# Kernel optimization log

Hardware: AMD Instinct MI355X
Metric: run time of the kernel (lower is better)

The kernel has to match this reference:

```python
import jax, jax.numpy as jnp
import numpy as np

N_NODES = 100000
N_EDGES = 1600000
N_GRAPHS = 64
DIMS = [(128, 128), (128, 128), (128, 64)]  # (in, out) per SAGEConv layer


def setup_inputs() -> dict:
    key = jax.random.key(0)
    ks = jax.random.split(key, 16)
    inp = {
        "x": jax.random.normal(ks[0], (N_NODES, DIMS[0][0]), dtype=jnp.float32),
        "edge_index": jax.random.randint(ks[1], (2, N_EDGES), 0, N_NODES, dtype=jnp.int64),
        "batch": jnp.sort(jax.random.randint(ks[2], (N_NODES,), 0, N_GRAPHS, dtype=jnp.int64)),
        "edge_attr": jax.random.normal(ks[3], (N_EDGES, 4), dtype=jnp.float32),
    }
    # SAGEConv params: lin_l (applied to mean-aggregated neighbors, has bias),
    # lin_r (applied to root/self features, no bias) -- PyG defaults.
    for i, (din, dout) in enumerate(DIMS):
        s = 1.0 / np.sqrt(din)
        inp[f"Wl{i}"] = jax.random.normal(ks[4 + 3 * i], (din, dout), dtype=jnp.float32) * s
        inp[f"Wr{i}"] = jax.random.normal(ks[5 + 3 * i], (din, dout), dtype=jnp.float32) * s
        inp[f"b{i}"] = jnp.zeros((dout,), dtype=jnp.float32)
    return inp


def _sage_conv(x, edge_index, Wl, Wr, b):
    # messages flow src -> dst (PyG source_to_target), mean aggregation at dst
    src, dst = edge_index[0], edge_index[1]
    msg = x[src]  # [E, F] gather
    agg = jax.ops.segment_sum(msg, dst, num_segments=x.shape[0])  # [N, F]
    deg = jax.ops.segment_sum(jnp.ones((src.shape[0],), x.dtype), dst, num_segments=x.shape[0])
    agg = agg / jnp.maximum(deg, 1.0)[:, None]  # mean; isolated nodes -> 0
    return agg @ Wl + x @ Wr + b


def reference(x, edge_index, batch, edge_attr, Wl0, Wr0, b0, Wl1, Wr1, b1, Wl2, Wr2, b2):
    del edge_attr  # cast to float in original, never used by SAGEConv
    h = x.astype(jnp.float32)
    params = [(Wl0, Wr0, b0), (Wl1, Wr1, b1), (Wl2, Wr2, b2)]
    for i, (Wl, Wr, b) in enumerate(params):
        h = _sage_conv(h, edge_index, Wl, Wr, b)
        if i < len(params) - 1:
            h = jax.nn.relu(h)  # dropout is identity in eval mode
    # global_mean_pool over graphs
    pooled = jax.ops.segment_sum(h, batch, num_segments=N_GRAPHS)
    counts = jax.ops.segment_sum(jnp.ones((h.shape[0],), h.dtype), batch, num_segments=N_GRAPHS)
    return pooled / jnp.maximum(counts, 1.0)[:, None]
```

## Files before the change

### kernel.cpp

```cpp
#include <hip/hip_runtime.h>
#include <hip/hip_bf16.h>

#define NN 100000
#define NE 1600000
#define NG 64
#define NBUK 782
#define ABLK 512
#define ACH 3125
#define PSPLIT 8

typedef short short8 __attribute__((ext_vector_type(8)));
typedef float f32x4 __attribute__((ext_vector_type(4)));
typedef float f32x2 __attribute__((ext_vector_type(2)));
typedef unsigned short ushort8v __attribute__((ext_vector_type(8)));
typedef unsigned int uint4v __attribute__((ext_vector_type(4)));
typedef unsigned int uint2v __attribute__((ext_vector_type(2)));

static inline int cdiv(int a, int b) { return (a + b - 1) / b; }

__device__ __forceinline__ short f2bf(float f) {
    return __builtin_bit_cast(short, __float2bfloat16(f));
}
__device__ __forceinline__ float bf2f(unsigned short u) {
    unsigned int x = ((unsigned int)u) << 16;
    return __builtin_bit_cast(float, x);
}

__global__ __launch_bounds__(256) void histA_kernel(const int* __restrict__ dst,
                                                    int* __restrict__ blockHist, int E) {
    __shared__ int h[NBUK];
    for (int i = threadIdx.x; i < NBUK; i += 256) h[i] = 0;
    __syncthreads();
    int base = blockIdx.x * ACH;
    int end = min(base + ACH, E);
    for (int e = base + threadIdx.x; e < end; e += 256) atomicAdd(&h[dst[e] >> 7], 1);
    __syncthreads();
    for (int i = threadIdx.x; i < NBUK; i += 256) blockHist[(size_t)i * ABLK + blockIdx.x] = h[i];
}

__global__ __launch_bounds__(512) void scanBlk_kernel(int* __restrict__ blockHist,
                                                      int* __restrict__ bucketTot) {
    __shared__ int s[ABLK];
    int b = blockIdx.x, t = threadIdx.x;
    int v = blockHist[(size_t)b * ABLK + t];
    s[t] = v;
    __syncthreads();
    for (int o = 1; o < ABLK; o <<= 1) {
        int u = (t >= o) ? s[t - o] : 0;
        __syncthreads();
        s[t] += u;
        __syncthreads();
    }
    blockHist[(size_t)b * ABLK + t] = s[t] - v;
    if (t == ABLK - 1) bucketTot[b] = s[ABLK - 1];
}

__global__ __launch_bounds__(1024) void scanTot_kernel(const int* __restrict__ bucketTot,
                                                       int* __restrict__ bucketBase,
                                                       int* __restrict__ off, int E) {
    __shared__ int s[1024];
    int t = threadIdx.x;
    int v = (t < NBUK) ? bucketTot[t] : 0;
    s[t] = v;
    __syncthreads();
    for (int o = 1; o < 1024; o <<= 1) {
        int u = (t >= o) ? s[t - o] : 0;
        __syncthreads();
        s[t] += u;
        __syncthreads();
    }
    if (t < NBUK) bucketBase[t] = s[t] - v;
    if (t == 0) {
        bucketBase[NBUK] = E;
        off[NN] = E;
    }
}

__global__ __launch_bounds__(256) void binA_kernel(const int* __restrict__ src,
                                                   const int* __restrict__ dst,
                                                   const int* __restrict__ blockHist,
                                                   const int* __restrict__ bucketBase,
                                                   int* __restrict__ binned, int E) {
    __shared__ int cur[NBUK];
    __shared__ int lbase[NBUK];
    for (int i = threadIdx.x; i < NBUK; i += 256) {
        cur[i] = 0;
        lbase[i] = bucketBase[i] + blockHist[(size_t)i * ABLK + blockIdx.x];
    }
    __syncthreads();
    int base = blockIdx.x * ACH;
    int end = min(base + ACH, E);
    for (int e = base + threadIdx.x; e < end; e += 256) {
        int d = dst[e];
        int b = d >> 7;
        int r = atomicAdd(&cur[b], 1);
        binned[lbase[b] + r] = src[e] | ((d & 127) << 20);
    }
}

__global__ __launch_bounds__(256) void bucketB_kernel(const int* __restrict__ binned,
                                                      const int* __restrict__ bucketBase,
                                                      int* __restrict__ csr,
                                                      int* __restrict__ off,
                                                      float* __restrict__ ideg, int N) {
    __shared__ int pair[2048];
    __shared__ int stage[4096];
    __shared__ int deg[128], loff[128], cur[128];
    int b = blockIdx.x, t = threadIdx.x;
    int e0 = bucketBase[b], e1 = bucketBase[b + 1];
    int cnt = e1 - e0;
    if (t < 128) deg[t] = 0;
    __syncthreads();
    for (int c0 = 0; c0 < cnt; c0 += 2048) {
        int cc = min(2048, cnt - c0);
        for (int i = t; i < cc; i += 256) pair[i] = binned[e0 + c0 + i];
        __syncthreads();
        for (int i = t; i < cc; i += 256) atomicAdd(&deg[pair[i] >> 20], 1);
        __syncthreads();
    }
    if (t < 128) loff[t] = deg[t];
    __syncthreads();
    for (int o = 1; o < 128; o <<= 1) {
        int u = (t < 128 && t >= o) ? loff[t - o] : 0;
        __syncthreads();
        if (t < 128) loff[t] += u;
        __syncthreads();
    }
    int nodeBase = b * 128;
    if (t < 128) {
        int ex = loff[t] - deg[t];
        cur[t] = ex;
        int n = nodeBase + t;
        if (n < N) {
            off[n] = e0 + ex;
            ideg[n] = 1.0f / (float)max(deg[t], 1);
        }
    }
    __syncthreads();
    if (cnt <= 4096) {
        for (int c0 = 0; c0 < cnt; c0 += 2048) {
            int cc = min(2048, cnt - c0);
            for (int i = t; i < cc; i += 256) pair[i] = binned[e0 + c0 + i];
            __syncthreads();
            for (int i = t; i < cc; i += 256) {
                int p = pair[i];
                int r = atomicAdd(&cur[p >> 20], 1);
                stage[r] = p & 0xFFFFF;
            }
            __syncthreads();
        }
        for (int i = t; i < cnt; i += 256) csr[e0 + i] = stage[i];
    } else {
        for (int c0 = 0; c0 < cnt; c0 += 2048) {
            int cc = min(2048, cnt - c0);
            for (int i = t; i < cc; i += 256) pair[i] = binned[e0 + c0 + i];
            __syncthreads();
            for (int i = t; i < cc; i += 256) {
                int p = pair[i];
                int r = atomicAdd(&cur[p >> 20], 1);
                csr[e0 + r] = p & 0xFFFFF;
            }
            __syncthreads();
        }
    }
}

__device__ __forceinline__ void wt_body(const float* Wl, const float* Wr, short* WT,
                                        int OUT, int idx) {
    int c = idx >> 7, k = idx & 127;
    float v = (c < OUT) ? Wl[k * OUT + c] : Wr[k * OUT + (c - OUT)];
    WT[idx] = f2bf(v);
}

__global__ __launch_bounds__(256) void setup_kernel(
    const float* __restrict__ x, short* __restrict__ xb,
    const float* __restrict__ Wl0, const float* __restrict__ Wr0, short* __restrict__ WT0,
    const float* __restrict__ Wl1, const float* __restrict__ Wr1, short* __restrict__ WT1,
    const float* __restrict__ Wl2, const float* __restrict__ Wr2, short* __restrict__ WT2,
    const int* __restrict__ batch, int* __restrict__ gstart) {
    int b = blockIdx.x;
    int tid = threadIdx.x;
    if (b < 6250) {
        int i = b * 256 + tid;
        const float4 v0 = ((const float4*)x)[i * 2];
        const float4 v1 = ((const float4*)x)[i * 2 + 1];
        short8 o;
        o[0] = f2bf(v0.x); o[1] = f2bf(v0.y); o[2] = f2bf(v0.z); o[3] = f2bf(v0.w);
        o[4] = f2bf(v1.x); o[5] = f2bf(v1.y); o[6] = f2bf(v1.z); o[7] = f2bf(v1.w);
        ((short8*)xb)[i] = o;
    } else if (b < 6378) {
        wt_body(Wl0, Wr0, WT0, 128, (b - 6250) * 256 + tid);
    } else if (b < 6506) {
        wt_body(Wl1, Wr1, WT1, 128, (b - 6378) * 256 + tid);
    } else if (b < 6570) {
        wt_body(Wl2, Wr2, WT2, 64, (b - 6506) * 256 + tid);
    } else {
        int n = (b - 6570) * 256 + tid;
        if (n >= NN) return;
        int g1 = batch[n];
        if (n == 0) {
            for (int g = 0; g <= g1; ++g) gstart[g] = 0;
        } else {
            int pb = batch[n - 1];
            for (int g = pb + 1; g <= g1; ++g) gstart[g] = n;
        }
        if (n == NN - 1) {
            for (int g = g1 + 1; g <= NG; ++g) gstart[g] = NN;
        }
    }
}

template <int OUT>
__global__ __launch_bounds__(256) void sage_gemm_mfma(
    const short* __restrict__ h, const short* __restrict__ WT,
    const float* __restrict__ bias,
    unsigned char* __restrict__ P, short* __restrict__ Q, int N) {
    constexpr int K = 128;
    constexpr int NT = OUT / 32;
    constexpr int WC = OUT / 2;
    constexpr int PWP = WC / 4 + 4;
    constexpr int PWQ = WC / 2 + 4;
    constexpr int LDSB = 32 * PWQ * 4;

    __shared__ char As[16384];
    __shared__ char eLds[4 * LDSB];

    const int tid = threadIdx.x;
    const int w = tid >> 6;
    const int lane = tid & 63;
    const int l15 = lane & 15;
    const int lhi = lane >> 4;
    const int rowBase = blockIdx.x * 64;
    const int colBase = w * WC;
    const bool isQ = (w >= 2);
    const int ocolBase = isQ ? colBase - OUT : colBase;
    char* myL = eLds + w * LDSB;

    {
        const char* gsrc = (const char*)(h + (size_t)rowBase * K);
#pragma unroll
        for (int p = 0; p < 4; ++p) {
            int lbase = (w * 4 + p) * 1024;
            int loff = lbase + lane * 16;
            int row = loff >> 8;
            int scol = (loff & 255) ^ ((row & 7) << 4);
            __builtin_amdgcn_global_load_lds(
                (const __attribute__((address_space(1))) unsigned int*)(gsrc + (size_t)row * 256 + scol),
                (__attribute__((address_space(3))) unsigned int*)(As + lbase),
                16, 0, 0);
        }
    }
    __syncthreads();

    f32x4 acc[4][NT];
#pragma unroll
    for (int mt = 0; mt < 4; ++mt)
#pragma unroll
        for (int nt = 0; nt < NT; ++nt) acc[mt][nt] = (f32x4){0.f, 0.f, 0.f, 0.f};

#pragma unroll
    for (int kt = 0; kt < 4; ++kt) {
        const int kb = kt * 64 + lhi * 16;
        short8 a[4], b[NT];
#pragma unroll
        for (int mt = 0; mt < 4; ++mt) {
            int row = mt * 16 + l15;
            a[mt] = *(const short8*)(As + row * 256 + (kb ^ ((row & 7) << 4)));
        }
#pragma unroll
        for (int nt = 0; nt < NT; ++nt)
            b[nt] = *(const short8*)(WT + (size_t)(colBase + nt * 16 + l15) * K + kt * 32 + lhi * 8);
#pragma unroll
        for (int mt = 0; mt < 4; ++mt)
#pragma unroll
            for (int nt = 0; nt < NT; ++nt)
                acc[mt][nt] = __builtin_amdgcn_mfma_f32_16x16x32_bf16(b[nt], a[mt], acc[mt][nt], 0, 0, 0);
    }

    if (!isQ) {
        constexpr int LPR = WC / 16;
        constexpr int RPP = 64 / LPR;
        constexpr int NP = 32 / RPP;
#pragma unroll
        for (int hh = 0; hh < 2; ++hh) {
#pragma unroll
            for (int mt2 = 0; mt2 < 2; ++mt2) {
                int mt = hh * 2 + mt2;
                int lr = mt2 * 16 + l15;
#pragma unroll
                for (int nt = 0; nt < NT; ++nt) {
                    unsigned u = (unsigned)__builtin_amdgcn_cvt_pk_fp8_f32(
                        acc[mt][nt][0], acc[mt][nt][1], 0, false);
                    u = (unsigned)__builtin_amdgcn_cvt_pk_fp8_f32(
                        acc[mt][nt][2], acc[mt][nt][3], (int)u, true);
                    *(unsigned*)(myL + (size_t)(lr * PWP + nt * 4 + lhi) * 4) = u;
                }
            }
#pragma unroll
            for (int p2 = 0; p2 < NP; ++p2) {
                int lr = p2 * RPP + lane / LPR;
                int wc = (lane % LPR) * 4;
                uint4v v = *(uint4v*)(myL + (size_t)(lr * PWP + wc) * 4);
                int grow = rowBase + hh * 32 + lr;
                if (grow < N)
                    *(uint4v*)(P + (size_t)grow * OUT + ocolBase + wc * 4) = v;
            }
        }
    } else {
        float4 bj[NT];
#pragma unroll
        for (int nt = 0; nt < NT; ++nt)
            bj[nt] = *(const float4*)(bias + ocolBase + nt * 16 + lhi * 4);
        constexpr int LPR = WC / 8;
        constexpr int RPP = 64 / LPR;
        constexpr int NP = 32 / RPP;
#pragma unroll
        for (int hh = 0; hh < 2; ++hh) {
#pragma unroll
            for (int mt2 = 0; mt2 < 2; ++mt2) {
                int mt = hh * 2 + mt2;
                int lr = mt2 * 16 + l15;
#pragma unroll
                for (int nt = 0; nt < NT; ++nt) {
                    float v0 = acc[mt][nt][0] + bj[nt].x;
                    float v1 = acc[mt][nt][1] + bj[nt].y;
                    float v2 = acc[mt][nt][2] + bj[nt].z;
                    float v3 = acc[mt][nt][3] + bj[nt].w;
                    unsigned lo = ((unsigned)(unsigned short)f2bf(v0)) |
                                  ((unsigned)(unsigned short)f2bf(v1) << 16);
                    unsigned hi = ((unsigned)(unsigned short)f2bf(v2)) |
                                  ((unsigned)(unsigned short)f2bf(v3) << 16);
                    uint2v u; u[0] = lo; u[1] = hi;
                    *(uint2v*)(myL + (size_t)(lr * PWQ + (nt * 4 + lhi) * 2) * 4) = u;
                }
            }
#pragma unroll
            for (int p2 = 0; p2 < NP; ++p2) {
                int lr = p2 * RPP + lane / LPR;
                int wc = (lane % LPR) * 4;
                uint4v v = *(uint4v*)(myL + (size_t)(lr * PWQ + wc) * 4);
                int grow = rowBase + hh * 32 + lr;
                if (grow < N)
                    *(uint4v*)((unsigned short*)Q + (size_t)grow * OUT + ocolBase + (lane % LPR) * 8) = v;
            }
        }
    }
}

template <int F, bool RELU>
__global__ __launch_bounds__(256) void gather_kernel(
    const int* __restrict__ csr, const int* __restrict__ off,
    const unsigned char* __restrict__ P, const float* __restrict__ ideg,
    const short* __restrict__ Qin, short* __restrict__ hout, int N) {
    constexpr int C = F / 16;
    int t = blockIdx.x * blockDim.x + threadIdx.x;
    int n = t / C, c = t % C;
    if (n >= N) return;
    int e0 = off[n], e1 = off[n + 1];
    const size_t cb = (size_t)c * 16;

    float f[16];
#pragma unroll
    for (int j = 0; j < 16; ++j) f[j] = 0.f;

    int e = e0;
    for (; e + 4 <= e1; e += 4) {
        int s0 = csr[e + 0], s1 = csr[e + 1], s2 = csr[e + 2], s3 = csr[e + 3];
        uint4v u0 = *(const uint4v*)(P + (size_t)s0 * F + cb);
        uint4v u1 = *(const uint4v*)(P + (size_t)s1 * F + cb);
        uint4v u2 = *(const uint4v*)(P + (size_t)s2 * F + cb);
        uint4v u3 = *(const uint4v*)(P + (size_t)s3 * F + cb);
#pragma unroll
        for (int wd = 0; wd < 4; ++wd) {
            f32x2 a0 = __builtin_amdgcn_cvt_pk_f32_fp8(u0[wd], false);
            f32x2 b0 = __builtin_amdgcn_cvt_pk_f32_fp8(u0[wd], true);
            f32x2 a1 = __builtin_amdgcn_cvt_pk_f32_fp8(u1[wd], false);
            f32x2 b1 = __builtin_amdgcn_cvt_pk_f32_fp8(u1[wd], true);
            f32x2 a2 = __builtin_amdgcn_cvt_pk_f32_fp8(u2[wd], false);
            f32x2 b2 = __builtin_amdgcn_cvt_pk_f32_fp8(u2[wd], true);
            f32x2 a3 = __builtin_amdgcn_cvt_pk_f32_fp8(u3[wd], false);
            f32x2 b3 = __builtin_amdgcn_cvt_pk_f32_fp8(u3[wd], true);
            f[wd * 4 + 0] += (a0[0] + a1[0]) + (a2[0] + a3[0]);
            f[wd * 4 + 1] += (a0[1] + a1[1]) + (a2[1] + a3[1]);
            f[wd * 4 + 2] += (b0[0] + b1[0]) + (b2[0] + b3[0]);
            f[wd * 4 + 3] += (b0[1] + b1[1]) + (b2[1] + b3[1]);
        }
    }
    for (; e < e1; ++e) {
        uint4v u = *(const uint4v*)(P + (size_t)csr[e] * F + cb);
#pragma unroll
        for (int wd = 0; wd < 4; ++wd) {
            f32x2 a = __builtin_amdgcn_cvt_pk_f32_fp8(u[wd], false);
            f32x2 b = __builtin_amdgcn_cvt_pk_f32_fp8(u[wd], true);
            f[wd * 4 + 0] += a[0];
            f[wd * 4 + 1] += a[1];
            f[wd * 4 + 2] += b[0];
            f[wd * 4 + 3] += b[1];
        }
    }

    float sc = ideg[n];
    const short* qp = Qin + (size_t)n * F + cb;
    ushort8v qa = *(const ushort8v*)qp, qb = *(const ushort8v*)(qp + 8);
    short8 oa, ob;
#pragma unroll
    for (int j = 0; j < 8; ++j) {
        float va = fmaf(f[j], sc, bf2f(qa[j]));
        float vb = fmaf(f[j + 8], sc, bf2f(qb[j]));
        if (RELU) { va = fmaxf(va, 0.f); vb = fmaxf(vb, 0.f); }
        oa[j] = f2bf(va);
        ob[j] = f2bf(vb);
    }
    short* op = hout + (size_t)n * F + cb;
    *(short8*)op = oa;
    *(short8*)(op + 8) = ob;
}

__global__ __launch_bounds__(256) void pool2_kernel(const unsigned short* __restrict__ h,
                                                    const int* __restrict__ gstart,
                                                    float* __restrict__ gpart) {
    int g = blockIdx.x / PSPLIT, part = blockIdx.x % PSPLIT;
    int s = gstart[g], e = gstart[g + 1];
    int cnt = e - s;
    int chunk = (cnt + PSPLIT - 1) / PSPLIT;
    int n0 = s + part * chunk;
    int n1 = min(n0 + chunk, e);
    int j = threadIdx.x & 63;
    int r = threadIdx.x >> 6;
    float acc = 0.f;
    for (int n = n0 + r; n < n1; n += 4) acc += bf2f(h[(size_t)n * 64 + j]);
    __shared__ float ls[256];
    ls[threadIdx.x] = acc;
    __syncthreads();
    if (threadIdx.x < 64) {
        float v = ls[threadIdx.x] + ls[threadIdx.x + 64] + ls[threadIdx.x + 128] + ls[threadIdx.x + 192];
        gpart[(size_t)(g * PSPLIT + part) * 64 + threadIdx.x] = v;
    }
}

__global__ void final_kernel(const float* __restrict__ gpart, const int* __restrict__ gstart,
                             float* __restrict__ out) {
    int t = blockIdx.x * blockDim.x + threadIdx.x;
    if (t >= NG * 64) return;
    int g = t >> 6, j = t & 63;
    float s = 0.f;
#pragma unroll
    for (int p = 0; p < PSPLIT; ++p) s += gpart[(size_t)(g * PSPLIT + p) * 64 + j];
    int cnt = gstart[g + 1] - gstart[g];
    out[t] = s / (float)max(cnt, 1);
}

extern "C" void kernel_launch(void* const* d_in, const int* in_sizes, int n_in,
                              void* d_out, int out_size, void* d_ws, size_t ws_size,
                              hipStream_t stream) {
    const float* x     = (const float*)d_in[0];
    const int*   ei    = (const int*)d_in[1];
    const int*   batch = (const int*)d_in[2];
    const float* Wl0 = (const float*)d_in[4];
    const float* Wr0 = (const float*)d_in[5];
    const float* b0  = (const float*)d_in[6];
    const float* Wl1 = (const float*)d_in[7];
    const float* Wr1 = (const float*)d_in[8];
    const float* b1  = (const float*)d_in[9];
    const float* Wl2 = (const float*)d_in[10];
    const float* Wr2 = (const float*)d_in[11];
    const float* b2  = (const float*)d_in[12];

    const int N = NN, E = NE;
    const int* src = ei;
    const int* dst = ei + E;

    const size_t HB = (size_t)NN * 128 * 2;
    char* ws = (char*)d_ws;
    short* xbf  = (short*)(ws);
    short* hA   = (short*)(ws + HB);
    short* hB   = (short*)(ws + 2 * HB);
    short* bufQ = (short*)(ws + 3 * HB);
    unsigned char* bufP = (unsigned char*)(ws + 4 * HB);
    char* p = ws + 4 * HB + (size_t)NN * 128;
    short* WT0  = (short*)p;        p += 256 * 128 * 2;
    short* WT1  = (short*)p;        p += 256 * 128 * 2;
    short* WT2  = (short*)p;        p += 128 * 128 * 2;
    float* ideg = (float*)p;        p += (size_t)N * 4;
    int* off    = (int*)p;          p += (size_t)(N + 4) * 4;
    int* blockHist = (int*)p;       p += (size_t)NBUK * ABLK * 4 + 16;
    int* bucketTot = (int*)p;       p += 784 * 4;
    int* bucketBase= (int*)p;       p += 784 * 4;
    int* gstart = (int*)p;          p += (NG + 2) * 4;
    float* gpart = (float*)p;       p += (size_t)NG * PSPLIT * 64 * 4;
    int* binned = (int*)p;          p += (size_t)E * 4;
    int* csr    = (int*)p;          p += (size_t)E * 4;

    histA_kernel<<<ABLK, 256, 0, stream>>>(dst, blockHist, E);
    scanBlk_kernel<<<NBUK, ABLK, 0, stream>>>(blockHist, bucketTot);
    scanTot_kernel<<<1, 1024, 0, stream>>>(bucketTot, bucketBase, off, E);
    binA_kernel<<<ABLK, 256, 0, stream>>>(src, dst, blockHist, bucketBase, binned, E);
    bucketB_kernel<<<NBUK, 256, 0, stream>>>(binned, bucketBase, csr, off, ideg, N);

    setup_kernel<<<6961, 256, 0, stream>>>(x, xbf, Wl0, Wr0, WT0, Wl1, Wr1, WT1,
                                           Wl2, Wr2, WT2, batch, gstart);

    const int GB = cdiv(N, 64);

    sage_gemm_mfma<128><<<GB, 256, 0, stream>>>(xbf, WT0, b0, bufP, bufQ, N);
    gather_kernel<128, true><<<cdiv(N * 8, 256), 256, 0, stream>>>(csr, off, bufP, ideg, bufQ, hA, N);
    sage_gemm_mfma<128><<<GB, 256, 0, stream>>>(hA, WT1, b1, bufP, bufQ, N);
    gather_kernel<128, true><<<cdiv(N * 8, 256), 256, 0, stream>>>(csr, off, bufP, ideg, bufQ, hB, N);
    sage_gemm_mfma<64><<<GB, 256, 0, stream>>>(hB, WT2, b2, bufP, bufQ, N);
    gather_kernel<64, false><<<cdiv(N * 4, 256), 256, 0, stream>>>(csr, off, bufP, ideg, bufQ, hA, N);

    pool2_kernel<<<NG * PSPLIT, 256, 0, stream>>>((const unsigned short*)hA, gstart, gpart);
    final_kernel<<<16, 256, 0, stream>>>(gpart, gstart, (float*)d_out);
}
```

Measured before the change: 243.7 us.

## Fuse histogram with setup kernel, double binning blocks, single-pass bucket sort

```diff
diff --git a/kernel.cpp b/kernel.cpp
--- a/kernel.cpp
+++ b/kernel.cpp
@@ -5,8 +5,8 @@
 #define NE 1600000
 #define NG 64
 #define NBUK 782
-#define ABLK 512
-#define ACH 3125
+#define ABLK 1024
+#define ACH 1563
 #define PSPLIT 8
 
 typedef short short8 __attribute__((ext_vector_type(8)));
@@ -26,20 +26,63 @@
     return __builtin_bit_cast(float, x);
 }
 
-__global__ __launch_bounds__(256) void histA_kernel(const int* __restrict__ dst,
-                                                    int* __restrict__ blockHist, int E) {
+__device__ __forceinline__ void wt_body(const float* Wl, const float* Wr, short* WT,
+                                        int OUT, int idx) {
+    int c = idx >> 7, k = idx & 127;
+    float v = (c < OUT) ? Wl[k * OUT + c] : Wr[k * OUT + (c - OUT)];
+    WT[idx] = f2bf(v);
+}
+
+__global__ __launch_bounds__(256) void hist_setup_kernel(
+    const int* __restrict__ dst, int* __restrict__ blockHist,
+    const float* __restrict__ x, short* __restrict__ xb,
+    const float* __restrict__ Wl0, const float* __restrict__ Wr0, short* __restrict__ WT0,
+    const float* __restrict__ Wl1, const float* __restrict__ Wr1, short* __restrict__ WT1,
+    const float* __restrict__ Wl2, const float* __restrict__ Wr2, short* __restrict__ WT2,
+    const int* __restrict__ batch, int* __restrict__ gstart, int E) {
     __shared__ int h[NBUK];
-    for (int i = threadIdx.x; i < NBUK; i += 256) h[i] = 0;
-    __syncthreads();
-    int base = blockIdx.x * ACH;
-    int end = min(base + ACH, E);
-    for (int e = base + threadIdx.x; e < end; e += 256) atomicAdd(&h[dst[e] >> 7], 1);
-    __syncthreads();
-    for (int i = threadIdx.x; i < NBUK; i += 256) blockHist[(size_t)i * ABLK + blockIdx.x] = h[i];
-}
-
-__global__ __launch_bounds__(512) void scanBlk_kernel(int* __restrict__ blockHist,
-                                                      int* __restrict__ bucketTot) {
+    int b = blockIdx.x;
+    int tid = threadIdx.x;
+    if (b < ABLK) {
+        for (int i = tid; i < NBUK; i += 256) h[i] = 0;
+        __syncthreads();
+        int base = b * ACH;
+        int end = min(base + ACH, E);
+        for (int e = base + tid; e < end; e += 256) atomicAdd(&h[dst[e] >> 7], 1);
+        __syncthreads();
+        for (int i = tid; i < NBUK; i += 256) blockHist[(size_t)i * ABLK + b] = h[i];
+    } else if (b < ABLK + 6250) {
+        int i = (b - ABLK) * 256 + tid;
+        const float4 v0 = ((const float4*)x)[i * 2];
+        const float4 v1 = ((const float4*)x)[i * 2 + 1];
+        short8 o;
+        o[0] = f2bf(v0.x); o[1] = f2bf(v0.y); o[2] = f2bf(v0.z); o[3] = f2bf(v0.w);
+        o[4] = f2bf(v1.x); o[5] = f2bf(v1.y); o[6] = f2bf(v1.z); o[7] = f2bf(v1.w);
+        ((short8*)xb)[i] = o;
+    } else if (b < ABLK + 6378) {
+        wt_body(Wl0, Wr0, WT0, 128, (b - ABLK - 6250) * 256 + tid);
+    } else if (b < ABLK + 6506) {
+        wt_body(Wl1, Wr1, WT1, 128, (b - ABLK - 6378) * 256 + tid);
+    } else if (b < ABLK + 6570) {
+        wt_body(Wl2, Wr2, WT2, 64, (b - ABLK - 6506) * 256 + tid);
+    } else {
+        int n = (b - ABLK - 6570) * 256 + tid;
+        if (n >= NN) return;
+        int g1 = batch[n];
+        if (n == 0) {
+            for (int g = 0; g <= g1; ++g) gstart[g] = 0;
+        } else {
+            int pb = batch[n - 1];
+            for (int g = pb + 1; g <= g1; ++g) gstart[g] = n;
+        }
+        if (n == NN - 1) {
+            for (int g = g1 + 1; g <= NG; ++g) gstart[g] = NN;
+        }
+    }
+}
+
+__global__ __launch_bounds__(1024) void scanBlk_kernel(int* __restrict__ blockHist,
+                                                       int* __restrict__ bucketTot) {
     __shared__ int s[ABLK];
     int b = blockIdx.x, t = threadIdx.x;
     int v = blockHist[(size_t)b * ABLK + t];
@@ -103,21 +146,23 @@
                                                       int* __restrict__ csr,
                                                       int* __restrict__ off,
                                                       float* __restrict__ ideg, int N) {
-    __shared__ int pair[2048];
+    __shared__ int pair[4096];
     __shared__ int stage[4096];
     __shared__ int deg[128], loff[128], cur[128];
     int b = blockIdx.x, t = threadIdx.x;
     int e0 = bucketBase[b], e1 = bucketBase[b + 1];
     int cnt = e1 - e0;
+    bool fits = (cnt <= 4096);
     if (t < 128) deg[t] = 0;
     __syncthreads();
-    for (int c0 = 0; c0 < cnt; c0 += 2048) {
-        int cc = min(2048, cnt - c0);
-        for (int i = t; i < cc; i += 256) pair[i] = binned[e0 + c0 + i];
-        __syncthreads();
-        for (int i = t; i < cc; i += 256) atomicAdd(&deg[pair[i] >> 20], 1);
-        __syncthreads();
-    }
+    if (fits) {
+        for (int i = t; i < cnt; i += 256) pair[i] = binned[e0 + i];
+        __syncthreads();
+        for (int i = t; i < cnt; i += 256) atomicAdd(&deg[pair[i] >> 20], 1);
+    } else {
+        for (int i = t; i < cnt; i += 256) atomicAdd(&deg[binned[e0 + i] >> 20], 1);
+    }
+    __syncthreads();
     if (t < 128) loff[t] = deg[t];
     __syncthreads();
     for (int o = 1; o < 128; o <<= 1) {
@@ -137,75 +182,19 @@
         }
     }
     __syncthreads();
-    if (cnt <= 4096) {
-        for (int c0 = 0; c0 < cnt; c0 += 2048) {
-            int cc = min(2048, cnt - c0);
-            for (int i = t; i < cc; i += 256) pair[i] = binned[e0 + c0 + i];
-            __syncthreads();
-            for (int i = t; i < cc; i += 256) {
-                int p = pair[i];
-                int r = atomicAdd(&cur[p >> 20], 1);
-                stage[r] = p & 0xFFFFF;
-            }
-            __syncthreads();
-        }
+    if (fits) {
+        for (int i = t; i < cnt; i += 256) {
+            int p = pair[i];
+            int r = atomicAdd(&cur[p >> 20], 1);
+            stage[r] = p & 0xFFFFF;
+        }
+        __syncthreads();
         for (int i = t; i < cnt; i += 256) csr[e0 + i] = stage[i];
     } else {
-        for (int c0 = 0; c0 < cnt; c0 += 2048) {
-            int cc = min(2048, cnt - c0);
-            for (int i = t; i < cc; i += 256) pair[i] = binned[e0 + c0 + i];
-            __syncthreads();
-            for (int i = t; i < cc; i += 256) {
-                int p = pair[i];
-                int r = atomicAdd(&cur[p >> 20], 1);
-                csr[e0 + r] = p & 0xFFFFF;
-            }
-            __syncthreads();
-        }
-    }
-}
-
-__device__ __forceinline__ void wt_body(const float* Wl, const float* Wr, short* WT,
-                                        int OUT, int idx) {
-    int c = idx >> 7, k = idx & 127;
-    float v = (c < OUT) ? Wl[k * OUT + c] : Wr[k * OUT + (c - OUT)];
-    WT[idx] = f2bf(v);
-}
-
-__global__ __launch_bounds__(256) void setup_kernel(
-    const float* __restrict__ x, short* __restrict__ xb,
-    const float* __restrict__ Wl0, const float* __restrict__ Wr0, short* __restrict__ WT0,
-    const float* __restrict__ Wl1, const float* __restrict__ Wr1, short* __restrict__ WT1,
-    const float* __restrict__ Wl2, const float* __restrict__ Wr2, short* __restrict__ WT2,
-    const int* __restrict__ batch, int* __restrict__ gstart) {
-    int b = blockIdx.x;
-    int tid = threadIdx.x;
-    if (b < 6250) {
-        int i = b * 256 + tid;
-        const float4 v0 = ((const float4*)x)[i * 2];
-        const float4 v1 = ((const float4*)x)[i * 2 + 1];
-        short8 o;
-        o[0] = f2bf(v0.x); o[1] = f2bf(v0.y); o[2] = f2bf(v0.z); o[3] = f2bf(v0.w);
-        o[4] = f2bf(v1.x); o[5] = f2bf(v1.y); o[6] = f2bf(v1.z); o[7] = f2bf(v1.w);
-        ((short8*)xb)[i] = o;
-    } else if (b < 6378) {
-        wt_body(Wl0, Wr0, WT0, 128, (b - 6250) * 256 + tid);
-    } else if (b < 6506) {
-        wt_body(Wl1, Wr1, WT1, 128, (b - 6378) * 256 + tid);
-    } else if (b < 6570) {
-        wt_body(Wl2, Wr2, WT2, 64, (b - 6506) * 256 + tid);
-    } else {
-        int n = (b - 6570) * 256 + tid;
-        if (n >= NN) return;
-        int g1 = batch[n];
-        if (n == 0) {
-            for (int g = 0; g <= g1; ++g) gstart[g] = 0;
-        } else {
-            int pb = batch[n - 1];
-            for (int g = pb + 1; g <= g1; ++g) gstart[g] = n;
-        }
-        if (n == NN - 1) {
-            for (int g = g1 + 1; g <= NG; ++g) gstart[g] = NN;
+        for (int i = t; i < cnt; i += 256) {
+            int p = binned[e0 + i];
+            int r = atomicAdd(&cur[p >> 20], 1);
+            csr[e0 + r] = p & 0xFFFFF;
         }
     }
 }
@@ -491,14 +480,13 @@
     int* binned = (int*)p;          p += (size_t)E * 4;
     int* csr    = (int*)p;          p += (size_t)E * 4;
 
-    histA_kernel<<<ABLK, 256, 0, stream>>>(dst, blockHist, E);
+    hist_setup_kernel<<<ABLK + 6961, 256, 0, stream>>>(
+        dst, blockHist, x, xbf, Wl0, Wr0, WT0, Wl1, Wr1, WT1, Wl2, Wr2, WT2,
+        batch, gstart, E);
     scanBlk_kernel<<<NBUK, ABLK, 0, stream>>>(blockHist, bucketTot);
     scanTot_kernel<<<1, 1024, 0, stream>>>(bucketTot, bucketBase, off, E);
     binA_kernel<<<ABLK, 256, 0, stream>>>(src, dst, blockHist, bucketBase, binned, E);
     bucketB_kernel<<<NBUK, 256, 0, stream>>>(binned, bucketBase, csr, off, ideg, N);
-
-    setup_kernel<<<6961, 256, 0, stream>>>(x, xbf, Wl0, Wr0, WT0, Wl1, Wr1, WT1,
-                                           Wl2, Wr2, WT2, batch, gstart);
 
     const int GB = cdiv(N, 64);
 
```

Result: slower. 249.0 us (+2.2%).
